# Kernel tuning notes

Measured on AMD Instinct MI355X. Metric: run time of the kernel, lower is better.

Reference implementation:

```python
import jax, jax.numpy as jnp
import numpy as np


def setup_inputs() -> dict:
    key = jax.random.key(0)
    k = jax.random.split(key, 5)
    B, S, D, W = 8, 2048, 128, 16
    H4 = 4 * D
    scale = 1.0 / np.sqrt(D)
    return {
        "x": jax.random.normal(k[0], (B, S, D), dtype=jnp.float32),
        "w_ih": jax.random.uniform(k[1], (H4, D), jnp.float32, -scale, scale),
        "w_hh": jax.random.uniform(k[2], (H4, D), jnp.float32, -scale, scale),
        "b_ih": jax.random.uniform(k[3], (H4,), jnp.float32, -scale, scale),
        "b_hh": jax.random.uniform(k[4], (H4,), jnp.float32, -scale, scale),
        "window_size": W,
    }


def reference(x, w_ih, w_hh, b_ih, b_hh, window_size):
    # x: (B, S, D). Build overlapping causal windows of length W, run an LSTM
    # over each window independently, take the final hidden state per window.
    B, S, D = x.shape
    W = window_size
    pad = jnp.zeros((B, W - 1, D), dtype=x.dtype)
    xp = jnp.concatenate([pad, x], axis=1)                     # (B, S+W-1, D)
    idx = jnp.arange(S)[:, None] + jnp.arange(W)[None, :]      # (S, W)
    win = xp[:, idx]                                           # (B, S, W, D)
    xf = win.reshape(B * S, W, D)                              # (N, W, D), N=B*S
    # Precompute input-gate projections for all timesteps at once.
    xg = jnp.einsum('nwd,gd->nwg', xf, w_ih) + b_ih            # (N, W, 4D)

    def step(carry, gx):
        h, c = carry
        g = gx + h @ w_hh.T + b_hh                             # (N, 4D)
        i, f, gg, o = jnp.split(g, 4, axis=-1)                 # PyTorch gate order i,f,g,o
        c = jax.nn.sigmoid(f) * c + jax.nn.sigmoid(i) * jnp.tanh(gg)
        h = jax.nn.sigmoid(o) * jnp.tanh(c)
        return (h, c), None

    h0 = jnp.zeros((B * S, D), dtype=x.dtype)
    (h, _), _ = jax.lax.scan(step, (h0, h0), jnp.swapaxes(xg, 0, 1))
    return h.reshape(B, S, D)
```

## Files before the change

kernel.cpp:

```cpp
#include <hip/hip_runtime.h>

typedef __attribute__((ext_vector_type(8))) short bf16x8;
typedef __attribute__((ext_vector_type(4))) float f32x4;
typedef __attribute__((ext_vector_type(4))) _Float16 f16x4;
typedef __attribute__((ext_vector_type(2))) unsigned int u32x2;

#define B_N 8
#define S_N 2048
#define D_N 128
#define W_N 16
#define G_N 512
#define CH 32
#define ROWS 47

#define L1 1.4426950408889634f
#define L2 2.8853900817779268f

__device__ __forceinline__ short f2bf(float f) {
  union { float f; unsigned u; } v; v.f = f;
  unsigned r = v.u + 0x7fffu + ((v.u >> 16) & 1u);
  return (short)(r >> 16);
}

__device__ __forceinline__ bf16x8 cvt8(const float* p) {
  f32x4 a = *(const f32x4*)p;
  f32x4 b = *(const f32x4*)(p + 4);
  bf16x8 v;
  v[0] = f2bf(a[0]); v[1] = f2bf(a[1]); v[2] = f2bf(a[2]); v[3] = f2bf(a[3]);
  v[4] = f2bf(b[0]); v[5] = f2bf(b[1]); v[6] = f2bf(b[2]); v[7] = f2bf(b[3]);
  return v;
}

__global__ void __launch_bounds__(512, 2)
fused_rnn(const float* __restrict__ x, const float* __restrict__ w_ih,
          const float* __restrict__ w_hh, const float* __restrict__ b_ih,
          const float* __restrict__ b_hh, float* __restrict__ out) {
  __shared__ char xg_s[ROWS * 1024];
  __shared__ char hbuf[2][CH * 256];

  const int tid  = threadIdx.x;
  const int lane = tid & 63;
  const int wv   = tid >> 6;
  const int lm   = lane & 15;
  const int q    = lane >> 4;
  const int n0   = blockIdx.x * CH;
  const int b    = n0 >> 11;
  const int s0   = n0 & (S_N - 1);

  bf16x8 wf[4][4];
#pragma unroll
  for (int i = 0; i < 4; ++i) {
    const int g = (wv + 8 * i) * 16 + lm;
#pragma unroll
    for (int kt = 0; kt < 4; ++kt)
      wf[i][kt] = cvt8(w_ih + g * D_N + kt * 32 + q * 8);
  }

  {
    f32x4 bias[4];
#pragma unroll
    for (int i = 0; i < 4; ++i) {
      const int g0 = (wv + 8 * i) * 16 + 4 * q;
      f32x4 bi = *(const f32x4*)(b_ih + g0);
      f32x4 bh = *(const f32x4*)(b_hh + g0);
      bias[i].x = bi.x + bh.x; bias[i].y = bi.y + bh.y;
      bias[i].z = bi.z + bh.z; bias[i].w = bi.w + bh.w;
    }

#pragma unroll
    for (int rg = 0; rg < 3; ++rg) {
      const int r = rg * 16 + lm;
      const int t = s0 - (W_N - 1) + r;
      int tc = t < 0 ? 0 : t;
      tc = tc < S_N - 1 ? tc : S_N - 1;
      const bool valid = (t >= 0);
      const float* xr = x + ((long)b * S_N + tc) * D_N;
      bf16x8 xf[4];
#pragma unroll
      for (int kt = 0; kt < 4; ++kt) {
        if (valid) xf[kt] = cvt8(xr + kt * 32 + q * 8);
        else { bf16x8 z; for (int e = 0; e < 8; ++e) z[e] = 0; xf[kt] = z; }
      }
      f32x4 acc[4] = {{0,0,0,0},{0,0,0,0},{0,0,0,0},{0,0,0,0}};
#pragma unroll
      for (int i = 0; i < 4; ++i)
#pragma unroll
        for (int kt = 0; kt < 4; ++kt)
          acc[i] = __builtin_amdgcn_mfma_f32_16x16x32_bf16(wf[i][kt], xf[kt], acc[i], 0, 0, 0);
      if (r < ROWS) {
#pragma unroll
        for (int i = 0; i < 4; ++i) {
          const int g0 = (wv + 8 * i) * 16 + 4 * q;
          const int byte = (r * 1024 + g0 * 2) ^ ((r & 7) << 4);
          f16x4 hv;
          hv[0] = (_Float16)(acc[i][0] + bias[i].x);
          hv[1] = (_Float16)(acc[i][1] + bias[i].y);
          hv[2] = (_Float16)(acc[i][2] + bias[i].z);
          hv[3] = (_Float16)(acc[i][3] + bias[i].w);
          *(f16x4*)(xg_s + byte) = hv;
        }
      }
    }
  }

#pragma unroll
  for (int i = 0; i < 4; ++i) {
    const int g = (wv + 8 * i) * 16 + lm;
#pragma unroll
    for (int kt = 0; kt < 4; ++kt)
      wf[i][kt] = cvt8(w_hh + g * D_N + kt * 32 + q * 8);
  }
  __syncthreads();

  const int swz = (lm & 7) << 4;
  const int wrb = (lm * 256 + (16 * wv + 4 * q) * 2) ^ swz;
  int rdb[4];
#pragma unroll
  for (int kt = 0; kt < 4; ++kt)
    rdb[kt] = (lm * 256 + kt * 64 + q * 16) ^ swz;

  f32x4 c[2] = {{0,0,0,0},{0,0,0,0}};

#pragma unroll
  for (int w = 0; w < W_N; ++w) {
#pragma unroll
    for (int cg = 0; cg < 2; ++cg) {
      const int row = cg * 16 + lm + w;
      f32x4 acc[4];
#pragma unroll
      for (int i = 0; i < 4; ++i) {
        const int g0 = (wv + 8 * i) * 16 + 4 * q;
        const int byte = (row * 1024 + g0 * 2) ^ ((row & 7) << 4);
        f16x4 xv = *(const f16x4*)(xg_s + byte);
        acc[i][0] = (float)xv[0]; acc[i][1] = (float)xv[1];
        acc[i][2] = (float)xv[2]; acc[i][3] = (float)xv[3];
      }

      if (w > 0) {
        const char* bb = hbuf[(w - 1) & 1] + cg * 4096;
#pragma unroll
        for (int kh = 0; kh < 2; ++kh) {
          bf16x8 hf0 = *(const bf16x8*)(bb + rdb[2 * kh]);
          bf16x8 hf1 = *(const bf16x8*)(bb + rdb[2 * kh + 1]);
#pragma unroll
          for (int i = 0; i < 4; ++i) {
            acc[i] = __builtin_amdgcn_mfma_f32_16x16x32_bf16(wf[i][2 * kh],     hf0, acc[i], 0, 0, 0);
            acc[i] = __builtin_amdgcn_mfma_f32_16x16x32_bf16(wf[i][2 * kh + 1], hf1, acc[i], 0, 0, 0);
          }
        }
      }

      float hr[4];
#pragma unroll
      for (int r = 0; r < 4; ++r) {
        float ei = __builtin_amdgcn_exp2f(-L1 * acc[0][r]);
        float ef = __builtin_amdgcn_exp2f(-L1 * acc[1][r]);
        float eg = __builtin_amdgcn_exp2f(-L2 * acc[2][r]);
        float a   = (1.0f + ei) * (1.0f + eg);
        float num = c[cg][r] * a + (1.0f - eg) * (1.0f + ef);
        float den = (1.0f + ef) * a;
        float cn  = num * __builtin_amdgcn_rcpf(den);
        c[cg][r] = cn;
        float eo = __builtin_amdgcn_exp2f(-L1 * acc[3][r]);
        float ec = __builtin_amdgcn_exp2f(-L2 * cn);
        hr[r] = (1.0f - ec) * __builtin_amdgcn_rcpf((1.0f + eo) * (1.0f + ec));
      }

      unsigned lo = ((unsigned)(unsigned short)f2bf(hr[0])) |
                    (((unsigned)(unsigned short)f2bf(hr[1])) << 16);
      unsigned hi = ((unsigned)(unsigned short)f2bf(hr[2])) |
                    (((unsigned)(unsigned short)f2bf(hr[3])) << 16);
      u32x2 v = {lo, hi};
      *(u32x2*)(&hbuf[w & 1][cg * 4096 + wrb]) = v;
    }
    __syncthreads();
  }

  {
    const int chain = tid >> 4;
    const int d0 = (tid & 15) * 8;
    const int byte = (chain * 256 + d0 * 2) ^ ((chain & 7) << 4);
    bf16x8 hv = *(const bf16x8*)(&hbuf[1][byte]);
    float* op = out + (long)(n0 + chain) * D_N + d0;
    f32x4 v0, v1;
#pragma unroll
    for (int e = 0; e < 4; ++e) {
      union { unsigned u; float f; } t0, t1;
      t0.u = ((unsigned)(unsigned short)hv[e]) << 16;
      t1.u = ((unsigned)(unsigned short)hv[4 + e]) << 16;
      v0[e] = t0.f; v1[e] = t1.f;
    }
    *(f32x4*)op = v0;
    *(f32x4*)(op + 4) = v1;
  }
}

extern "C" void kernel_launch(void* const* d_in, const int* in_sizes, int n_in,
                              void* d_out, int out_size, void* d_ws, size_t ws_size,
                              hipStream_t stream) {
  const float* x    = (const float*)d_in[0];
  const float* w_ih = (const float*)d_in[1];
  const float* w_hh = (const float*)d_in[2];
  const float* b_ih = (const float*)d_in[3];
  const float* b_hh = (const float*)d_in[4];
  float* out = (float*)d_out;

  fused_rnn<<<(B_N * S_N) / CH, 512, 0, stream>>>(x, w_ih, w_hh, b_ih, b_hh, out);
}
```

Baseline: 159.5 us.

## Double windows per block and prefetch next-step gate inputs into registers

Raises the number of windows per block from 32 to 64, so the overlapping input projection covers 80 rows per 64 windows instead of 47 rows per 32 windows, cutting redundant x·W_ih work and the w_ih/w_hh weight reloads per window. The recurrent loop now handles four chain groups per wave and software-pipelines the shared-memory load of the next timestep's gate inputs into a double-buffered register array. In exchange, shared memory per block roughly doubles (about 112 KB), which likely allows only one resident block per CU instead of two. The grid halves, and the extra live registers risk spilling under the existing launch bounds.

Result: faster. 141.3 us (-11.4%).

```diff
diff --git a/kernel.cpp b/kernel.cpp
--- a/kernel.cpp
+++ b/kernel.cpp
@@ -10,8 +10,8 @@
 #define D_N 128
 #define W_N 16
 #define G_N 512
-#define CH 32
-#define ROWS 47
+#define CH 64
+#define ROWS 80
 
 #define L1 1.4426950408889634f
 #define L2 2.8853900817779268f
@@ -68,7 +68,7 @@
     }
 
 #pragma unroll
-    for (int rg = 0; rg < 3; ++rg) {
+    for (int rg = 0; rg < 5; ++rg) {
       const int r = rg * 16 + lm;
       const int t = s0 - (W_N - 1) + r;
       int tc = t < 0 ? 0 : t;
@@ -87,18 +87,16 @@
 #pragma unroll
         for (int kt = 0; kt < 4; ++kt)
           acc[i] = __builtin_amdgcn_mfma_f32_16x16x32_bf16(wf[i][kt], xf[kt], acc[i], 0, 0, 0);
-      if (r < ROWS) {
-#pragma unroll
-        for (int i = 0; i < 4; ++i) {
-          const int g0 = (wv + 8 * i) * 16 + 4 * q;
-          const int byte = (r * 1024 + g0 * 2) ^ ((r & 7) << 4);
-          f16x4 hv;
-          hv[0] = (_Float16)(acc[i][0] + bias[i].x);
-          hv[1] = (_Float16)(acc[i][1] + bias[i].y);
-          hv[2] = (_Float16)(acc[i][2] + bias[i].z);
-          hv[3] = (_Float16)(acc[i][3] + bias[i].w);
-          *(f16x4*)(xg_s + byte) = hv;
-        }
+#pragma unroll
+      for (int i = 0; i < 4; ++i) {
+        const int g0 = (wv + 8 * i) * 16 + 4 * q;
+        const int byte = (r * 1024 + g0 * 2) ^ ((r & 7) << 4);
+        f16x4 hv;
+        hv[0] = (_Float16)(acc[i][0] + bias[i].x);
+        hv[1] = (_Float16)(acc[i][1] + bias[i].y);
+        hv[2] = (_Float16)(acc[i][2] + bias[i].z);
+        hv[3] = (_Float16)(acc[i][3] + bias[i].w);
+        *(f16x4*)(xg_s + byte) = hv;
       }
     }
   }
@@ -119,21 +117,41 @@
   for (int kt = 0; kt < 4; ++kt)
     rdb[kt] = (lm * 256 + kt * 64 + q * 16) ^ swz;
 
-  f32x4 c[2] = {{0,0,0,0},{0,0,0,0}};
+  f32x4 c[4] = {{0,0,0,0},{0,0,0,0},{0,0,0,0},{0,0,0,0}};
+  f16x4 xv[2][4][4];
+
+#pragma unroll
+  for (int cg = 0; cg < 4; ++cg) {
+    const int row = cg * 16 + lm;
+#pragma unroll
+    for (int i = 0; i < 4; ++i) {
+      const int g0 = (wv + 8 * i) * 16 + 4 * q;
+      const int byte = (row * 1024 + g0 * 2) ^ ((row & 7) << 4);
+      xv[0][cg][i] = *(const f16x4*)(xg_s + byte);
+    }
+  }
 
 #pragma unroll
   for (int w = 0; w < W_N; ++w) {
-#pragma unroll
-    for (int cg = 0; cg < 2; ++cg) {
-      const int row = cg * 16 + lm + w;
+    const int cur = w & 1, nxt = cur ^ 1;
+#pragma unroll
+    for (int cg = 0; cg < 4; ++cg) {
+      if (w < W_N - 1) {
+        const int rown = cg * 16 + lm + w + 1;
+#pragma unroll
+        for (int i = 0; i < 4; ++i) {
+          const int g0 = (wv + 8 * i) * 16 + 4 * q;
+          const int byte = (rown * 1024 + g0 * 2) ^ ((rown & 7) << 4);
+          xv[nxt][cg][i] = *(const f16x4*)(xg_s + byte);
+        }
+      }
+
       f32x4 acc[4];
 #pragma unroll
       for (int i = 0; i < 4; ++i) {
-        const int g0 = (wv + 8 * i) * 16 + 4 * q;
-        const int byte = (row * 1024 + g0 * 2) ^ ((row & 7) << 4);
-        f16x4 xv = *(const f16x4*)(xg_s + byte);
-        acc[i][0] = (float)xv[0]; acc[i][1] = (float)xv[1];
-        acc[i][2] = (float)xv[2]; acc[i][3] = (float)xv[3];
+        f16x4 t = xv[cur][cg][i];
+        acc[i][0] = (float)t[0]; acc[i][1] = (float)t[1];
+        acc[i][2] = (float)t[2]; acc[i][3] = (float)t[3];
       }
 
       if (w > 0) {
@@ -171,14 +189,16 @@
       unsigned hi = ((unsigned)(unsigned short)f2bf(hr[2])) |
                     (((unsigned)(unsigned short)f2bf(hr[3])) << 16);
       u32x2 v = {lo, hi};
-      *(u32x2*)(&hbuf[w & 1][cg * 4096 + wrb]) = v;
+      *(u32x2*)(&hbuf[cur][cg * 4096 + wrb]) = v;
     }
     __syncthreads();
   }
 
-  {
-    const int chain = tid >> 4;
-    const int d0 = (tid & 15) * 8;
+#pragma unroll
+  for (int p = 0; p < 2; ++p) {
+    const int idx = p * 512 + tid;
+    const int chain = idx >> 4;
+    const int d0 = (idx & 15) * 8;
     const int byte = (chain * 256 + d0 * 2) ^ ((chain & 7) << 4);
     bf16x8 hv = *(const bf16x8*)(&hbuf[1][byte]);
     float* op = out + (long)(n0 + chain) * D_N + d0;
```
